# Performance work log

Hardware: AMD Instinct MI355X
Metric: run time of the kernel (lower is better)

## Reference

```python
import jax, jax.numpy as jnp
import numpy as np

DIM = 256
N_EMBED = 8192
BETA = 0.25


def setup_inputs() -> dict:
    key = jax.random.key(0)
    k1, k2, k3, k4 = jax.random.split(key, 4)
    inp = {
        "input": jax.random.normal(k1, (16, 1024, DIM), dtype=jnp.float32),
        # nn.Embedding weight init: normal(0, dim**-0.5)
        "embed_weight": jax.random.normal(k2, (N_EMBED, DIM), dtype=jnp.float32) * (DIM ** -0.5),
        # nn.Linear(dim, dim): weight [out, in], bias [out]
        "proj_w": jax.random.normal(k3, (DIM, DIM), dtype=jnp.float32) * (DIM ** -0.5),
        "proj_b": jax.random.normal(k4, (DIM,), dtype=jnp.float32) * 0.01,
    }
    return inp


def reference(input, embed_weight, proj_w, proj_b):
    flatten = input.reshape(-1, DIM)                      # [N, d]
    # projected codebook: Linear(embedding.weight)
    quant_codebook = embed_weight @ proj_w.T + proj_b     # [K, d]
    d = (jnp.sum(flatten ** 2, axis=1, keepdims=True)
         + jnp.sum(quant_codebook ** 2, axis=1)
         - 2.0 * jnp.einsum('nd,kd->nk', flatten, quant_codebook))  # [N, K]
    min_encoding_indices = jnp.argmin(d, axis=1)          # [N]
    z_quantize = quant_codebook[min_encoding_indices].reshape(input.shape)
    sg = jax.lax.stop_gradient
    diff = jnp.mean((sg(z_quantize) - input) ** 2)
    commit_loss = jnp.mean((z_quantize - sg(input)) ** 2)
    diff = diff + BETA * commit_loss                      # legacy=True branch
    # straight-through estimator
    z_quantize = input + sg(z_quantize - input)
    return (z_quantize, diff, min_encoding_indices)
```

## Files before the change

### kernel.cpp

```cpp
#include <hip/hip_runtime.h>

#define DIMD   256
#define NTOK   16384
#define NCODE  8192
#define NELEM  (NTOK * DIMD)

#define PBM 64
#define PBK 128
#define BD 32
#define PAD 4
#define SA (PBM + PAD)
#define SB (PBK + PAD)

#define MARGIN 0.5f
#define EBUF_CAP 1024

#define CODES_PER_BLOCK 1024
#define TOK_PER_BLOCK   256
#define MIN_NGROUPS (CODES_PER_BLOCK / 16)
#define EM_SPLITS 2
#define EM_CPW (NCODE / EM_SPLITS / 4)
#define EM_NGROUPS (EM_CPW / 16)

#define PROJ_BLOCKS ((NCODE / PBM) * (DIMD / PBK))
#define CONV_BLOCKS (NTOK / 4)

typedef float floatx4 __attribute__((ext_vector_type(4)));
typedef short short8  __attribute__((ext_vector_type(8)));
typedef unsigned int u32;

__device__ __forceinline__ unsigned short f2bf(float f) {
    unsigned u = __float_as_uint(f);
    unsigned r = (u + 0x7FFFu + ((u >> 16) & 1u)) >> 16;
    return (unsigned short)r;
}

__device__ __forceinline__ void gl_lds16(const void* g, void* l) {
    __builtin_amdgcn_global_load_lds(
        (const __attribute__((address_space(1))) u32*)g,
        (__attribute__((address_space(3))) u32*)l, 16, 0, 0);
}

__device__ __forceinline__ unsigned fkey(float f) {
    unsigned u = __float_as_uint(f);
    return (u & 0x80000000u) ? ~u : (u | 0x80000000u);
}
__device__ __forceinline__ float funkey(unsigned k) {
    unsigned u = (k & 0x80000000u) ? (k & 0x7FFFFFFFu) : ~k;
    return __uint_as_float(u);
}

__device__ __forceinline__ size_t cb2_idx(int row, int col) {
    return ((size_t)((row >> 4) * 8 + (col >> 5))) * 512
         + (size_t)((((col >> 3) & 3) * 16 + (row & 15)) * 8 + (col & 7));
}

__global__ __launch_bounds__(256, 3)
void prep_kernel(const float* __restrict__ E, const float* __restrict__ W,
                 const float* __restrict__ bias, float* __restrict__ C,
                 unsigned short* __restrict__ Cb2,
                 float* __restrict__ cnormA, float* __restrict__ cnormB,
                 const float* __restrict__ X, float* __restrict__ xnorm,
                 unsigned short* __restrict__ Xb,
                 unsigned long long* __restrict__ fin,
                 unsigned* __restrict__ minkey,
                 unsigned* __restrict__ cnt, float* __restrict__ out)
{
    __shared__ float smem[BD * SA + BD * SB];

    const int bid = blockIdx.x;
    const int tid = threadIdx.x;

    if (bid >= PROJ_BLOCKS) {
        const int row0 = (bid - PROJ_BLOCKS) * 4;
        const int wave = tid >> 6;
        const int lane = tid & 63;
        const int row  = row0 + wave;
        float4 v = *(const float4*)&X[(size_t)row * DIMD + lane * 4];
        ushort4 h = {f2bf(v.x), f2bf(v.y), f2bf(v.z), f2bf(v.w)};
        *(ushort4*)&Xb[(size_t)row * DIMD + lane * 4] = h;
        float s = v.x * v.x + v.y * v.y + v.z * v.z + v.w * v.w;
#pragma unroll
        for (int off = 1; off < 64; off <<= 1) s += __shfl_xor(s, off);
        if (lane == 0) xnorm[row] = s;
        if (tid < 4) {
            fin[row0 + tid]    = ~0ull;
            minkey[row0 + tid] = ~0u;
        }
        if (bid == PROJ_BLOCKS && tid == 0) { *cnt = 0; out[NELEM] = 0.f; }
        return;
    }

    float* As = smem;
    float* Bs = smem + BD * SA;

    const int tx  = tid & 15;
    const int ty  = tid >> 4;
    const int m0  = (bid & 127) * PBM;
    const int j0  = (bid >> 7) * PBK;

    const int srow = tid >> 3;
    const int scol = (tid & 7) * 4;

    float acc[4][8];
#pragma unroll
    for (int i = 0; i < 4; ++i)
#pragma unroll
        for (int j = 0; j < 8; ++j) acc[i][j] = 0.f;

    for (int dc = 0; dc < DIMD / BD; ++dc) {
        const int d0 = dc * BD;
        __syncthreads();
#pragma unroll
        for (int rr = 0; rr < 2; ++rr) {
            const int r = srow + rr * 32;
            float4 av = *(const float4*)&E[(size_t)(m0 + r) * DIMD + d0 + scol];
            As[(scol + 0) * SA + r] = av.x;
            As[(scol + 1) * SA + r] = av.y;
            As[(scol + 2) * SA + r] = av.z;
            As[(scol + 3) * SA + r] = av.w;
        }
#pragma unroll
        for (int rr = 0; rr < 4; ++rr) {
            const int r = srow + rr * 32;
            float4 bv = *(const float4*)&W[(size_t)(j0 + r) * DIMD + d0 + scol];
            Bs[(scol + 0) * SB + r] = bv.x;
            Bs[(scol + 1) * SB + r] = bv.y;
            Bs[(scol + 2) * SB + r] = bv.z;
            Bs[(scol + 3) * SB + r] = bv.w;
        }
        __syncthreads();
#pragma unroll 4
        for (int d = 0; d < BD; ++d) {
            float4 a0 = *(float4*)&As[d * SA + ty * 4];
            float4 b0 = *(float4*)&Bs[d * SB + tx * 4];
            float4 b1 = *(float4*)&Bs[d * SB + 64 + tx * 4];
            float a[4] = {a0.x, a0.y, a0.z, a0.w};
            float b[8] = {b0.x, b0.y, b0.z, b0.w, b1.x, b1.y, b1.z, b1.w};
#pragma unroll
            for (int i = 0; i < 4; ++i)
#pragma unroll
                for (int j = 0; j < 8; ++j) acc[i][j] = fmaf(a[i], b[j], acc[i][j]);
        }
    }

    __syncthreads();
    float* red = smem;

    float4 bja = *(const float4*)&bias[j0 + tx * 4];
    float4 bjb = *(const float4*)&bias[j0 + 64 + tx * 4];
#pragma unroll
    for (int i = 0; i < 4; ++i) {
        const int mloc = ty * 4 + i;
        const int row  = m0 + mloc;
        const size_t rbase = (size_t)row * DIMD;
        float o[8] = {acc[i][0] + bja.x, acc[i][1] + bja.y, acc[i][2] + bja.z, acc[i][3] + bja.w,
                      acc[i][4] + bjb.x, acc[i][5] + bjb.y, acc[i][6] + bjb.z, acc[i][7] + bjb.w};
        *(float4*)&C[rbase + j0 + tx * 4]      = *(float4*)&o[0];
        *(float4*)&C[rbase + j0 + 64 + tx * 4] = *(float4*)&o[4];
        ushort4 h0 = {f2bf(o[0]), f2bf(o[1]), f2bf(o[2]), f2bf(o[3])};
        ushort4 h1 = {f2bf(o[4]), f2bf(o[5]), f2bf(o[6]), f2bf(o[7])};
        *(ushort4*)&Cb2[cb2_idx(row, j0 + tx * 4)]      = h0;
        *(ushort4*)&Cb2[cb2_idx(row, j0 + 64 + tx * 4)] = h1;
        float p = 0.f;
#pragma unroll
        for (int j = 0; j < 8; ++j) p = fmaf(o[j], o[j], p);
        red[mloc * 16 + tx] = p;
    }
    __syncthreads();
    if (tid < 64) {
        float s = 0.f;
#pragma unroll
        for (int k = 0; k < 16; ++k) s += red[tid * 16 + k];
        float* dst = (j0 == 0) ? cnormA : cnormB;
        dst[m0 + tid] = s;
    }
}

__global__ __launch_bounds__(256, 2)
void dist_min_kernel(const unsigned short* __restrict__ Xb,
                     const unsigned short* __restrict__ Cb2,
                     const float* __restrict__ cnormA,
                     const float* __restrict__ cnormB,
                     unsigned* __restrict__ minkey)
{
    __shared__ short Bls[2][4096];
    __shared__ float cnl[CODES_PER_BLOCK];

    const int tid  = threadIdx.x;
    const int lane = tid & 63;
    const int wv   = tid >> 6;
    const int l15  = lane & 15;
    const int quad = lane >> 4;
    const int tok0 = blockIdx.x * TOK_PER_BLOCK + wv * 64;
    const int cbase = blockIdx.y * CODES_PER_BLOCK;

    {
        const int t4 = tid * 4;
        float4 va = *(const float4*)&cnormA[cbase + t4];
        float4 vb = *(const float4*)&cnormB[cbase + t4];
        cnl[t4 + 0] = va.x + vb.x;
        cnl[t4 + 1] = va.y + vb.y;
        cnl[t4 + 2] = va.z + vb.z;
        cnl[t4 + 3] = va.w + vb.w;
    }

    const unsigned short* bsrc = Cb2 + (size_t)cbase * DIMD;
    auto STAGE = [&](int g) {
        const unsigned short* s = bsrc + (size_t)g * 4096 + wv * 1024 + lane * 8;
        short* d = &Bls[g & 1][wv * 1024];
        gl_lds16(s,       d);
        gl_lds16(s + 512, d + 512);
    };
    STAGE(0);
    STAGE(1);

    short8 a[4][8];
#pragma unroll
    for (int i = 0; i < 4; ++i) {
        const unsigned short* ap = Xb + (size_t)(tok0 + i * 16 + l15) * DIMD + quad * 8;
#pragma unroll
        for (int ks = 0; ks < 8; ++ks)
            a[i][ks] = *(const short8*)(ap + ks * 32);
    }

    float runv[16];
#pragma unroll
    for (int s = 0; s < 16; ++s) runv[s] = 3.4e38f;

    __syncthreads();

    for (int g = 0; g < MIN_NGROUPS; ++g) {
        const short* bp = &Bls[g & 1][lane * 8];
        short8 bc[8];
#pragma unroll
        for (int ks = 0; ks < 8; ++ks) bc[ks] = *(const short8*)(bp + ks * 512);
        const float cnc = cnl[g * 16 + l15];

        floatx4 acc[4];
#pragma unroll
        for (int i = 0; i < 4; ++i) acc[i] = (floatx4){0.f, 0.f, 0.f, 0.f};
#pragma unroll
        for (int ks = 0; ks < 8; ++ks)
#pragma unroll
            for (int i = 0; i < 4; ++i)
                acc[i] = __builtin_amdgcn_mfma_f32_16x16x32_bf16(a[i][ks], bc[ks], acc[i], 0, 0, 0);

#pragma unroll
        for (int i = 0; i < 4; ++i)
#pragma unroll
            for (int r = 0; r < 4; ++r)
                runv[i * 4 + r] = fminf(runv[i * 4 + r], fmaf(-2.f, acc[i][r], cnc));

        __syncthreads();
        if (g + 2 < MIN_NGROUPS) STAGE(g + 2);
    }

#pragma unroll
    for (int s = 0; s < 16; ++s) {
        float m = runv[s];
#pragma unroll
        for (int off = 1; off < 16; off <<= 1) m = fminf(m, __shfl_xor(m, off));
        runv[s] = m;
    }
    if (l15 == 0) {
#pragma unroll
        for (int i = 0; i < 4; ++i)
#pragma unroll
            for (int r = 0; r < 4; ++r)
                atomicMin(&minkey[tok0 + i * 16 + quad * 4 + r], fkey(runv[i * 4 + r]));
    }
}

__global__ __launch_bounds__(256, 2)
void dist_emit_kernel(const unsigned short* __restrict__ Xb,
                      const unsigned short* __restrict__ Cb2,
                      const float* __restrict__ cnormA,
                      const float* __restrict__ cnormB,
                      const unsigned* __restrict__ minkey,
                      unsigned* __restrict__ list, unsigned* __restrict__ count,
                      unsigned cap)
{
    __shared__ float tokthr[64];
    __shared__ unsigned ebuf[EBUF_CAP];
    __shared__ unsigned ecnt, gbase;

    const int tid  = threadIdx.x;
    const int lane = tid & 63;
    const int wv   = tid >> 6;
    const int l15  = lane & 15;
    const int quad = lane >> 4;
    const int tok0 = blockIdx.x * 64;
    const int cbase = blockIdx.y * (NCODE / EM_SPLITS) + wv * EM_CPW;

    if (tid == 0) ecnt = 0;
    if (tid < 64) tokthr[tid] = funkey(minkey[tok0 + tid]) + MARGIN;
    __syncthreads();

    short8 a[4][8];
#pragma unroll
    for (int i = 0; i < 4; ++i) {
        const unsigned short* ap = Xb + (size_t)(tok0 + i * 16 + l15) * DIMD + quad * 8;
#pragma unroll
        for (int ks = 0; ks < 8; ++ks)
            a[i][ks] = *(const short8*)(ap + ks * 32);
    }

    float thr[16];
#pragma unroll
    for (int i = 0; i < 4; ++i)
#pragma unroll
        for (int r = 0; r < 4; ++r)
            thr[i * 4 + r] = tokthr[i * 16 + quad * 4 + r];

    const unsigned short* bp0 = Cb2 + (size_t)cbase * DIMD + lane * 8;

    short8 breg[2][8];
    float  cnr[2];
#pragma unroll
    for (int ks = 0; ks < 8; ++ks) breg[0][ks] = *(const short8*)(bp0 + ks * 512);
    cnr[0] = cnormA[cbase + l15] + cnormB[cbase + l15];

    auto group_body = [&](int g, short8 (&bc)[8], short8 (&bn)[8],
                          float cnc, float& cnn) {
        const int code0 = cbase + g * 16;
        if (g + 1 < EM_NGROUPS) {
            const unsigned short* bpn = bp0 + (size_t)(g + 1) * 4096;
#pragma unroll
            for (int ks = 0; ks < 8; ++ks) bn[ks] = *(const short8*)(bpn + ks * 512);
            const int cnx = code0 + 16 + l15;
            cnn = cnormA[cnx] + cnormB[cnx];
        }

        floatx4 acc[4];
#pragma unroll
        for (int i = 0; i < 4; ++i) acc[i] = (floatx4){0.f, 0.f, 0.f, 0.f};
#pragma unroll
        for (int ks = 0; ks < 8; ++ks)
#pragma unroll
            for (int i = 0; i < 4; ++i)
                acc[i] = __builtin_amdgcn_mfma_f32_16x16x32_bf16(a[i][ks], bc[ks], acc[i], 0, 0, 0);

        unsigned mask = 0;
#pragma unroll
        for (int i = 0; i < 4; ++i)
#pragma unroll
            for (int r = 0; r < 4; ++r) {
                const float dd = fmaf(-2.f, acc[i][r], cnc);
                if (dd < thr[i * 4 + r]) mask |= (1u << (i * 4 + r));
            }

        if (__any(mask != 0)) {
            if (mask) {
                unsigned pos = atomicAdd(&ecnt, (unsigned)__popc(mask));
#pragma unroll
                for (int i = 0; i < 4; ++i)
#pragma unroll
                    for (int r = 0; r < 4; ++r) {
                        const int s = i * 4 + r;
                        if (mask & (1u << s)) {
                            const unsigned token = tok0 + i * 16 + quad * 4 + r;
                            const unsigned entry = (token << 13) | (unsigned)(code0 + l15);
                            if (pos < EBUF_CAP) ebuf[pos] = entry;
                            else { unsigned gp = atomicAdd(count, 1u); if (gp < cap) list[gp] = entry; }
                            ++pos;
                        }
                    }
            }
        }
    };

    for (int gg = 0; gg < EM_NGROUPS; gg += 2) {
        group_body(gg,     breg[0], breg[1], cnr[0], cnr[1]);
        group_body(gg + 1, breg[1], breg[0], cnr[1], cnr[0]);
    }

    __syncthreads();
    const unsigned n = (ecnt < EBUF_CAP) ? ecnt : EBUF_CAP;
    if (tid == 0) gbase = atomicAdd(count, n);
    __syncthreads();
    const unsigned gb = gbase;
    for (unsigned i = tid; i < n; i += 256) {
        const unsigned p = gb + i;
        if (p < cap) list[p] = ebuf[i];
    }
}

__global__ __launch_bounds__(256)
void rescore_kernel(const float* __restrict__ X, const float* __restrict__ C,
                    const float* __restrict__ xnorm,
                    const float* __restrict__ cnormA,
                    const float* __restrict__ cnormB,
                    const unsigned* __restrict__ list, const unsigned* __restrict__ count,
                    unsigned cap, unsigned long long* __restrict__ fin)
{
    const int lane = threadIdx.x & 63;
    const int g16  = lane & 15;
    const int sub  = lane >> 4;
    const int gid  = ((blockIdx.x * 256 + threadIdx.x) >> 6) * 4 + sub;
    const int ng   = ((gridDim.x * 256) >> 6) * 4;
    unsigned n = *count; if (n > cap) n = cap;

    for (unsigned c = gid; c < n; c += ng) {
        const unsigned e = list[c];
        const unsigned tok = e >> 13, code = e & 8191u;
        const float* xr = &X[(size_t)tok * DIMD];
        const float* cr = &C[(size_t)code * DIMD];
        float dot = 0.f;
#pragma unroll
        for (int r = 0; r < 4; ++r) {
            float4 x4 = *(const float4*)&xr[r * 64 + g16 * 4];
            float4 c4 = *(const float4*)&cr[r * 64 + g16 * 4];
            dot = fmaf(x4.x, c4.x, dot);
            dot = fmaf(x4.y, c4.y, dot);
            dot = fmaf(x4.z, c4.z, dot);
            dot = fmaf(x4.w, c4.w, dot);
        }
#pragma unroll
        for (int d = 1; d < 16; d <<= 1) dot += __shfl_xor(dot, d);
        if (g16 == 0) {
            const float dd = xnorm[tok] + (cnormA[code] + cnormB[code]) - 2.f * dot;
            const unsigned long long p =
                ((unsigned long long)__float_as_uint(dd) << 32) | code;
            atomicMin(&fin[tok], p);
        }
    }
}

__global__ __launch_bounds__(256)
void finalize_kernel(const float* __restrict__ X, const float* __restrict__ C,
                     const unsigned long long* __restrict__ fin,
                     float* __restrict__ out)
{
    __shared__ float part[4];
    const int lane = threadIdx.x & 63;
    const int wv   = threadIdx.x >> 6;
    const int t0   = blockIdx.x * 64;

    float local = 0.f;
    for (int it = 0; it < 16; ++it) {
        const int t = t0 + wv * 16 + it;
        const unsigned code = (unsigned)(fin[t] & 0xFFFFFFFFull);
        float4 c4 = *(const float4*)&C[(size_t)code * DIMD + lane * 4];
        float4 x4 = *(const float4*)&X[(size_t)t * DIMD + lane * 4];
        float4 w  = {c4.x - x4.x, c4.y - x4.y, c4.z - x4.z, c4.w - x4.w};
        local += w.x * w.x + w.y * w.y + w.z * w.z + w.w * w.w;
        float4 zq = {x4.x + w.x, x4.y + w.y, x4.z + w.z, x4.w + w.w};
        *(float4*)&out[(size_t)t * DIMD + lane * 4] = zq;
        if (lane == 0) out[NELEM + 1 + t] = (float)code;
    }
#pragma unroll
    for (int off = 1; off < 64; off <<= 1) local += __shfl_xor(local, off);
    if (lane == 0) part[wv] = local;
    __syncthreads();
    if (threadIdx.x == 0) {
        const float s = part[0] + part[1] + part[2] + part[3];
        atomicAdd(&out[NELEM], s * (1.25f / (float)NELEM));
    }
}

extern "C" void kernel_launch(void* const* d_in, const int* in_sizes, int n_in,
                              void* d_out, int out_size, void* d_ws, size_t ws_size,
                              hipStream_t stream)
{
    const float* X = (const float*)d_in[0];
    const float* E = (const float*)d_in[1];
    const float* W = (const float*)d_in[2];
    const float* b = (const float*)d_in[3];
    float* out = (float*)d_out;

    char* w = (char*)d_ws;
    float* C            = (float*)w;           w += (size_t)NCODE * DIMD * 4;
    unsigned short* Xb  = (unsigned short*)w;  w += (size_t)NTOK * DIMD * 2;
    unsigned short* Cb2 = (unsigned short*)w;  w += (size_t)NCODE * DIMD * 2;
    float* xnorm        = (float*)w;           w += (size_t)NTOK * 4;
    float* cnormA       = (float*)w;           w += (size_t)NCODE * 4;
    float* cnormB       = (float*)w;           w += (size_t)NCODE * 4;
    unsigned* cnt       = (unsigned*)w;        w += 256;
    unsigned long long* fin = (unsigned long long*)w; w += (size_t)NTOK * 8;
    unsigned* minkey    = (unsigned*)w;        w += (size_t)NTOK * 4;
    unsigned* list      = (unsigned*)w;

    size_t used = (size_t)(w - (char*)d_ws);
    size_t avail = (ws_size > used) ? (ws_size - used) / 4 : 0;
    unsigned cap = (unsigned)((avail > 16777216u) ? 16777216u : avail);

    prep_kernel<<<PROJ_BLOCKS + CONV_BLOCKS, 256, 0, stream>>>(
        E, W, b, C, Cb2, cnormA, cnormB, X, xnorm, Xb, fin, minkey, cnt, out);
    dist_min_kernel<<<dim3(NTOK / TOK_PER_BLOCK, NCODE / CODES_PER_BLOCK), 256, 0, stream>>>(
        Xb, Cb2, cnormA, cnormB, minkey);
    dist_emit_kernel<<<dim3(NTOK / 64, EM_SPLITS), 256, 0, stream>>>(
        Xb, Cb2, cnormA, cnormB, minkey, list, cnt, cap);
    rescore_kernel<<<1024, 256, 0, stream>>>(X, C, xnorm, cnormA, cnormB, list, cnt, cap, fin);
    finalize_kernel<<<NTOK / 64, 256, 0, stream>>>(X, C, fin, out);
}
```

Baseline: 267.3 us.

## Fuse fp32 rescoring of candidates into the emit kernel, dropping global list

Candidates kept in the emit kernel's shared buffer are now rescored in exact fp32 inside the same block and merged into the per-token result with an atomic min. The global candidate list, its counter and the separate rescore kernel are removed. This saves one launch and the global write and read of the list. In exchange the rescoring runs on only 16 groups per block, and any overflow past the shared buffer is rescored by a slow serial per-thread loop.

```diff
diff --git a/kernel.cpp b/kernel.cpp
--- a/kernel.cpp
+++ b/kernel.cpp
@@ -63,8 +63,7 @@
                  const float* __restrict__ X, float* __restrict__ xnorm,
                  unsigned short* __restrict__ Xb,
                  unsigned long long* __restrict__ fin,
-                 unsigned* __restrict__ minkey,
-                 unsigned* __restrict__ cnt, float* __restrict__ out)
+                 unsigned* __restrict__ minkey, float* __restrict__ out)
 {
     __shared__ float smem[BD * SA + BD * SB];
 
@@ -87,7 +86,7 @@
             fin[row0 + tid]    = ~0ull;
             minkey[row0 + tid] = ~0u;
         }
-        if (bid == PROJ_BLOCKS && tid == 0) { *cnt = 0; out[NELEM] = 0.f; }
+        if (bid == PROJ_BLOCKS && tid == 0) out[NELEM] = 0.f;
         return;
     }
 
@@ -278,12 +277,13 @@
                       const float* __restrict__ cnormA,
                       const float* __restrict__ cnormB,
                       const unsigned* __restrict__ minkey,
-                      unsigned* __restrict__ list, unsigned* __restrict__ count,
-                      unsigned cap)
+                      const float* __restrict__ X, const float* __restrict__ C,
+                      const float* __restrict__ xnorm,
+                      unsigned long long* __restrict__ fin)
 {
     __shared__ float tokthr[64];
     __shared__ unsigned ebuf[EBUF_CAP];
-    __shared__ unsigned ecnt, gbase;
+    __shared__ unsigned ecnt;
 
     const int tid  = threadIdx.x;
     const int lane = tid & 63;
@@ -360,9 +360,18 @@
                         const int s = i * 4 + r;
                         if (mask & (1u << s)) {
                             const unsigned token = tok0 + i * 16 + quad * 4 + r;
-                            const unsigned entry = (token << 13) | (unsigned)(code0 + l15);
-                            if (pos < EBUF_CAP) ebuf[pos] = entry;
-                            else { unsigned gp = atomicAdd(count, 1u); if (gp < cap) list[gp] = entry; }
+                            const unsigned codeX = (unsigned)(code0 + l15);
+                            if (pos < EBUF_CAP) {
+                                ebuf[pos] = (token << 13) | codeX;
+                            } else {
+                                const float* xr = &X[(size_t)token * DIMD];
+                                const float* cr = &C[(size_t)codeX * DIMD];
+                                float dot = 0.f;
+                                for (int d = 0; d < DIMD; ++d) dot = fmaf(xr[d], cr[d], dot);
+                                const float ddf = xnorm[token] + (cnormA[codeX] + cnormB[codeX]) - 2.f * dot;
+                                atomicMin(&fin[token],
+                                          ((unsigned long long)__float_as_uint(ddf) << 32) | codeX);
+                            }
                             ++pos;
                         }
                     }
@@ -377,32 +386,10 @@
 
     __syncthreads();
     const unsigned n = (ecnt < EBUF_CAP) ? ecnt : EBUF_CAP;
-    if (tid == 0) gbase = atomicAdd(count, n);
-    __syncthreads();
-    const unsigned gb = gbase;
-    for (unsigned i = tid; i < n; i += 256) {
-        const unsigned p = gb + i;
-        if (p < cap) list[p] = ebuf[i];
-    }
-}
-
-__global__ __launch_bounds__(256)
-void rescore_kernel(const float* __restrict__ X, const float* __restrict__ C,
-                    const float* __restrict__ xnorm,
-                    const float* __restrict__ cnormA,
-                    const float* __restrict__ cnormB,
-                    const unsigned* __restrict__ list, const unsigned* __restrict__ count,
-                    unsigned cap, unsigned long long* __restrict__ fin)
-{
-    const int lane = threadIdx.x & 63;
-    const int g16  = lane & 15;
-    const int sub  = lane >> 4;
-    const int gid  = ((blockIdx.x * 256 + threadIdx.x) >> 6) * 4 + sub;
-    const int ng   = ((gridDim.x * 256) >> 6) * 4;
-    unsigned n = *count; if (n > cap) n = cap;
-
-    for (unsigned c = gid; c < n; c += ng) {
-        const unsigned e = list[c];
+    const int g16 = lane & 15;
+    const int grp = wv * 4 + (lane >> 4);
+    for (unsigned c = grp; c < n; c += 16) {
+        const unsigned e = ebuf[c];
         const unsigned tok = e >> 13, code = e & 8191u;
         const float* xr = &X[(size_t)tok * DIMD];
         const float* cr = &C[(size_t)code * DIMD];
@@ -476,21 +463,15 @@
     float* xnorm        = (float*)w;           w += (size_t)NTOK * 4;
     float* cnormA       = (float*)w;           w += (size_t)NCODE * 4;
     float* cnormB       = (float*)w;           w += (size_t)NCODE * 4;
-    unsigned* cnt       = (unsigned*)w;        w += 256;
     unsigned long long* fin = (unsigned long long*)w; w += (size_t)NTOK * 8;
     unsigned* minkey    = (unsigned*)w;        w += (size_t)NTOK * 4;
-    unsigned* list      = (unsigned*)w;
-
-    size_t used = (size_t)(w - (char*)d_ws);
-    size_t avail = (ws_size > used) ? (ws_size - used) / 4 : 0;
-    unsigned cap = (unsigned)((avail > 16777216u) ? 16777216u : avail);
+    (void)ws_size;
 
     prep_kernel<<<PROJ_BLOCKS + CONV_BLOCKS, 256, 0, stream>>>(
-        E, W, b, C, Cb2, cnormA, cnormB, X, xnorm, Xb, fin, minkey, cnt, out);
+        E, W, b, C, Cb2, cnormA, cnormB, X, xnorm, Xb, fin, minkey, out);
     dist_min_kernel<<<dim3(NTOK / TOK_PER_BLOCK, NCODE / CODES_PER_BLOCK), 256, 0, stream>>>(
         Xb, Cb2, cnormA, cnormB, minkey);
     dist_emit_kernel<<<dim3(NTOK / 64, EM_SPLITS), 256, 0, stream>>>(
-        Xb, Cb2, cnormA, cnormB, minkey, list, cnt, cap);
-    rescore_kernel<<<1024, 256, 0, stream>>>(X, C, xnorm, cnormA, cnormB, list, cnt, cap, fin);
+        Xb, Cb2, cnormA, cnormB, minkey, X, C, xnorm, fin);
     finalize_kernel<<<NTOK / 64, 256, 0, stream>>>(X, C, fin, out);
 }
```

Measured after the change: 339.8 us. +27.1%, slower.

## Switch dist_min to 32x32x16 bf16 MFMA with a new codebook layout

Applied to the files above, without the earlier changes.

The distance-min kernel moves from 16x16x32 MFMA tiles (each wave covering 64 tokens × 16 codes) to 32x32x16 MFMA tiles (each wave covering 32 tokens × 32 codes). The prep kernel now also writes a second bf16 codebook copy (Cb3) laid out for the 32x32 operand pattern. Blocks shrink to 128 tokens, stage 32 codes per group, and declare 4 blocks per CU in the launch bounds. The goal is more MFMA work per LDS operand load and fewer instructions per flop. The cost is an extra codebook write, doubled LDS staging buffers and a wider 32-lane shuffle reduction.

```diff
diff --git a/kernel.cpp b/kernel.cpp
--- a/kernel.cpp
+++ b/kernel.cpp
@@ -16,8 +16,8 @@
 #define EBUF_CAP 1024
 
 #define CODES_PER_BLOCK 1024
-#define TOK_PER_BLOCK   256
-#define MIN_NGROUPS (CODES_PER_BLOCK / 16)
+#define MIN_TOKB 128
+#define MIN_NGROUPS (CODES_PER_BLOCK / 32)
 #define EM_SPLITS 2
 #define EM_CPW (NCODE / EM_SPLITS / 4)
 #define EM_NGROUPS (EM_CPW / 16)
@@ -25,8 +25,9 @@
 #define PROJ_BLOCKS ((NCODE / PBM) * (DIMD / PBK))
 #define CONV_BLOCKS (NTOK / 4)
 
-typedef float floatx4 __attribute__((ext_vector_type(4)));
-typedef short short8  __attribute__((ext_vector_type(8)));
+typedef float floatx4  __attribute__((ext_vector_type(4)));
+typedef float floatx16 __attribute__((ext_vector_type(16)));
+typedef short short8   __attribute__((ext_vector_type(8)));
 typedef unsigned int u32;
 
 __device__ __forceinline__ unsigned short f2bf(float f) {
@@ -55,10 +56,15 @@
          + (size_t)((((col >> 3) & 3) * 16 + (row & 15)) * 8 + (col & 7));
 }
 
+__device__ __forceinline__ size_t cb3_idx(int row, int col) {
+    return ((size_t)((row >> 5) * 16 + (col >> 4))) * 512
+         + (size_t)((((col >> 3) & 1) * 32 + (row & 31)) * 8 + (col & 7));
+}
+
 __global__ __launch_bounds__(256, 3)
 void prep_kernel(const float* __restrict__ E, const float* __restrict__ W,
                  const float* __restrict__ bias, float* __restrict__ C,
-                 unsigned short* __restrict__ Cb2,
+                 unsigned short* __restrict__ Cb2, unsigned short* __restrict__ Cb3,
                  float* __restrict__ cnormA, float* __restrict__ cnormB,
                  const float* __restrict__ X, float* __restrict__ xnorm,
                  unsigned short* __restrict__ Xb,
@@ -162,6 +168,8 @@
         ushort4 h1 = {f2bf(o[4]), f2bf(o[5]), f2bf(o[6]), f2bf(o[7])};
         *(ushort4*)&Cb2[cb2_idx(row, j0 + tx * 4)]      = h0;
         *(ushort4*)&Cb2[cb2_idx(row, j0 + 64 + tx * 4)] = h1;
+        *(ushort4*)&Cb3[cb3_idx(row, j0 + tx * 4)]      = h0;
+        *(ushort4*)&Cb3[cb3_idx(row, j0 + 64 + tx * 4)] = h1;
         float p = 0.f;
 #pragma unroll
         for (int j = 0; j < 8; ++j) p = fmaf(o[j], o[j], p);
@@ -177,22 +185,22 @@
     }
 }
 
-__global__ __launch_bounds__(256, 2)
+__global__ __launch_bounds__(256, 4)
 void dist_min_kernel(const unsigned short* __restrict__ Xb,
-                     const unsigned short* __restrict__ Cb2,
+                     const unsigned short* __restrict__ Cb3,
                      const float* __restrict__ cnormA,
                      const float* __restrict__ cnormB,
                      unsigned* __restrict__ minkey)
 {
-    __shared__ short Bls[2][4096];
+    __shared__ short Bls[2][8192];
     __shared__ float cnl[CODES_PER_BLOCK];
 
     const int tid  = threadIdx.x;
     const int lane = tid & 63;
     const int wv   = tid >> 6;
-    const int l15  = lane & 15;
-    const int quad = lane >> 4;
-    const int tok0 = blockIdx.x * TOK_PER_BLOCK + wv * 64;
+    const int col  = lane & 31;
+    const int half = lane >> 5;
+    const int tok0 = blockIdx.x * MIN_TOKB + wv * 32;
     const int cbase = blockIdx.y * CODES_PER_BLOCK;
 
     {
@@ -205,70 +213,61 @@
         cnl[t4 + 3] = va.w + vb.w;
     }
 
-    const unsigned short* bsrc = Cb2 + (size_t)cbase * DIMD;
+    const unsigned short* bsrc = Cb3 + (size_t)cbase * DIMD;
     auto STAGE = [&](int g) {
-        const unsigned short* s = bsrc + (size_t)g * 4096 + wv * 1024 + lane * 8;
-        short* d = &Bls[g & 1][wv * 1024];
-        gl_lds16(s,       d);
-        gl_lds16(s + 512, d + 512);
+        const unsigned short* s = bsrc + (size_t)g * 8192 + wv * 2048 + lane * 8;
+        short* d = &Bls[g & 1][wv * 2048];
+#pragma unroll
+        for (int c = 0; c < 4; ++c)
+            gl_lds16(s + c * 512, d + c * 512);
     };
     STAGE(0);
     STAGE(1);
 
-    short8 a[4][8];
-#pragma unroll
-    for (int i = 0; i < 4; ++i) {
-        const unsigned short* ap = Xb + (size_t)(tok0 + i * 16 + l15) * DIMD + quad * 8;
-#pragma unroll
-        for (int ks = 0; ks < 8; ++ks)
-            a[i][ks] = *(const short8*)(ap + ks * 32);
+    short8 a[16];
+    {
+        const unsigned short* ap = Xb + (size_t)(tok0 + col) * DIMD + half * 8;
+#pragma unroll
+        for (int ks = 0; ks < 16; ++ks)
+            a[ks] = *(const short8*)(ap + ks * 16);
     }
 
     float runv[16];
 #pragma unroll
-    for (int s = 0; s < 16; ++s) runv[s] = 3.4e38f;
+    for (int r = 0; r < 16; ++r) runv[r] = 3.4e38f;
 
     __syncthreads();
 
     for (int g = 0; g < MIN_NGROUPS; ++g) {
         const short* bp = &Bls[g & 1][lane * 8];
-        short8 bc[8];
-#pragma unroll
-        for (int ks = 0; ks < 8; ++ks) bc[ks] = *(const short8*)(bp + ks * 512);
-        const float cnc = cnl[g * 16 + l15];
-
-        floatx4 acc[4];
-#pragma unroll
-        for (int i = 0; i < 4; ++i) acc[i] = (floatx4){0.f, 0.f, 0.f, 0.f};
-#pragma unroll
-        for (int ks = 0; ks < 8; ++ks)
-#pragma unroll
-            for (int i = 0; i < 4; ++i)
-                acc[i] = __builtin_amdgcn_mfma_f32_16x16x32_bf16(a[i][ks], bc[ks], acc[i], 0, 0, 0);
-
-#pragma unroll
-        for (int i = 0; i < 4; ++i)
-#pragma unroll
-            for (int r = 0; r < 4; ++r)
-                runv[i * 4 + r] = fminf(runv[i * 4 + r], fmaf(-2.f, acc[i][r], cnc));
+        floatx16 acc = (floatx16)(0.f);
+#pragma unroll
+        for (int ks = 0; ks < 16; ++ks) {
+            short8 bc = *(const short8*)(bp + ks * 512);
+            acc = __builtin_amdgcn_mfma_f32_32x32x16_bf16(a[ks], bc, acc, 0, 0, 0);
+        }
+        const float cnc = cnl[g * 32 + col];
+#pragma unroll
+        for (int r = 0; r < 16; ++r)
+            runv[r] = fminf(runv[r], fmaf(-2.f, acc[r], cnc));
 
         __syncthreads();
         if (g + 2 < MIN_NGROUPS) STAGE(g + 2);
     }
 
 #pragma unroll
-    for (int s = 0; s < 16; ++s) {
-        float m = runv[s];
-#pragma unroll
-        for (int off = 1; off < 16; off <<= 1) m = fminf(m, __shfl_xor(m, off));
-        runv[s] = m;
-    }
-    if (l15 == 0) {
-#pragma unroll
-        for (int i = 0; i < 4; ++i)
-#pragma unroll
-            for (int r = 0; r < 4; ++r)
-                atomicMin(&minkey[tok0 + i * 16 + quad * 4 + r], fkey(runv[i * 4 + r]));
+    for (int r = 0; r < 16; ++r) {
+        float m = runv[r];
+#pragma unroll
+        for (int off = 1; off < 32; off <<= 1) m = fminf(m, __shfl_xor(m, off));
+        runv[r] = m;
+    }
+    if (col == 0) {
+#pragma unroll
+        for (int r = 0; r < 16; ++r) {
+            const int tok = tok0 + (r & 3) + 8 * (r >> 2) + 4 * half;
+            atomicMin(&minkey[tok], fkey(runv[r]));
+        }
     }
 }
 
@@ -473,6 +472,7 @@
     float* C            = (float*)w;           w += (size_t)NCODE * DIMD * 4;
     unsigned short* Xb  = (unsigned short*)w;  w += (size_t)NTOK * DIMD * 2;
     unsigned short* Cb2 = (unsigned short*)w;  w += (size_t)NCODE * DIMD * 2;
+    unsigned short* Cb3 = (unsigned short*)w;  w += (size_t)NCODE * DIMD * 2;
     float* xnorm        = (float*)w;           w += (size_t)NTOK * 4;
     float* cnormA       = (float*)w;           w += (size_t)NCODE * 4;
     float* cnormB       = (float*)w;           w += (size_t)NCODE * 4;
@@ -486,9 +486,9 @@
     unsigned cap = (unsigned)((avail > 16777216u) ? 16777216u : avail);
 
     prep_kernel<<<PROJ_BLOCKS + CONV_BLOCKS, 256, 0, stream>>>(
-        E, W, b, C, Cb2, cnormA, cnormB, X, xnorm, Xb, fin, minkey, cnt, out);
-    dist_min_kernel<<<dim3(NTOK / TOK_PER_BLOCK, NCODE / CODES_PER_BLOCK), 256, 0, stream>>>(
-        Xb, Cb2, cnormA, cnormB, minkey);
+        E, W, b, C, Cb2, Cb3, cnormA, cnormB, X, xnorm, Xb, fin, minkey, cnt, out);
+    dist_min_kernel<<<dim3(NTOK / MIN_TOKB, NCODE / CODES_PER_BLOCK), 256, 0, stream>>>(
+        Xb, Cb3, cnormA, cnormB, minkey);
     dist_emit_kernel<<<dim3(NTOK / 64, EM_SPLITS), 256, 0, stream>>>(
         Xb, Cb2, cnormA, cnormB, minkey, list, cnt, cap);
     rescore_kernel<<<1024, 256, 0, stream>>>(X, C, xnorm, cnormA, cnormB, list, cnt, cap, fin);
```

Result: no change. 266.8 us (-0.2%).
